# Kernel optimization log

Measured on AMD Instinct MI355X. Metric: run time of the kernel, lower is better.

Reference implementation:

```python
import jax, jax.numpy as jnp
import numpy as np

N = 100_000      # nodes
E = 1_200_000    # edges (before self-loops)
F_IN = 128       # num_node_features
G = 256          # number of graphs in the batch
C = 10           # num_classes
NEG_SLOPE = 0.2  # PyG GATConv default


def setup_inputs() -> dict:
    key = jax.random.key(0)
    ks = jax.random.split(key, 20)
    x = jax.random.normal(ks[0], (N, F_IN), jnp.float32)
    edge_index = jax.random.randint(ks[1], (2, E), 0, N, dtype=jnp.int32)
    # sorted graph assignment covering all G graphs (no empty segments)
    batch = (jnp.arange(N, dtype=jnp.int32) * G) // N

    def lin(k, fi, fo):
        return jax.random.normal(k, (fi, fo), jnp.float32) * (1.0 / np.sqrt(fi))

    dims = [(F_IN, 16), (16, 32), (32, 64)]
    params = {}
    for i, (fi, fo) in enumerate(dims, start=1):
        params[f"W{i}"] = lin(ks[3 * i], fi, fo)
        params[f"a{i}_src"] = jax.random.normal(ks[3 * i + 1], (fo,), jnp.float32) * 0.1
        params[f"a{i}_dst"] = jax.random.normal(ks[3 * i + 2], (fo,), jnp.float32) * 0.1
        params[f"b{i}"] = jnp.zeros((fo,), jnp.float32)
    params["fc_w"] = lin(ks[15], 64, C)
    params["fc_b"] = jnp.zeros((C,), jnp.float32)
    return {"x": x, "edge_index": edge_index, "batch": batch, **params}


def _gat_layer(x, src, dst, W, a_src, a_dst, b):
    # h = Theta x; e_ij = LeakyReLU(a_src.h_j + a_dst.h_i), softmax over dst i
    h = x @ W                                     # [N, F]
    s = h @ a_src                                 # [N]
    d = h @ a_dst                                 # [N]
    logits = jax.nn.leaky_relu(s[src] + d[dst], NEG_SLOPE)   # [E+N]
    m = jax.ops.segment_max(logits, dst, num_segments=N)     # per-dst max
    ex = jnp.exp(logits - m[dst])
    denom = jax.ops.segment_sum(ex, dst, num_segments=N)
    alpha = ex / (denom[dst] + 1e-16)             # [E+N]
    out = jax.ops.segment_sum(alpha[:, None] * h[src], dst, num_segments=N)
    return out + b


def reference(x, edge_index, batch, W1, a1_src, a1_dst, b1, W2, a2_src, a2_dst, b2,
              W3, a3_src, a3_dst, b3, fc_w, fc_b):
    # add self-loops (PyG GATConv default) -> every dst segment non-empty
    loops = jnp.arange(N, dtype=edge_index.dtype)
    src = jnp.concatenate([edge_index[0], loops])
    dst = jnp.concatenate([edge_index[1], loops])

    h = jax.nn.relu(_gat_layer(x, src, dst, W1, a1_src, a1_dst, b1))
    # F.dropout(training=False) is a no-op in eval
    h = jax.nn.relu(_gat_layer(h, src, dst, W2, a2_src, a2_dst, b2))
    h = jax.nn.relu(_gat_layer(h, src, dst, W3, a3_src, a3_dst, b3))
    pooled = jax.ops.segment_max(h, batch, num_segments=G)   # global_max_pool [G, 64]
    logits = pooled @ fc_w + fc_b
    return jax.nn.log_softmax(logits, axis=1)
```

## Files before the change

kernel.cpp:

```cpp
#include <hip/hip_runtime.h>
#include <hip/hip_bf16.h>
#include <hip/hip_fp16.h>
#include <math.h>

#define NEG_SLOPE 0.2f
#define NCHUNK 1024
#define BSHIFT 9
#define BNODES 512

__device__ __forceinline__ float leaky(float x) { return x > 0.f ? x : NEG_SLOPE * x; }
__device__ __forceinline__ int usan(int v, int n) { return ((unsigned)v < (unsigned)n) ? v : 0; }

__global__ void chunk_hist(const int* __restrict__ dst, int E, int Ec, int nbuck,
                           int* __restrict__ hmatT) {
    extern __shared__ int hist[];
    int c = blockIdx.x;
    for (int b = threadIdx.x; b < nbuck; b += 256) hist[b] = 0;
    __syncthreads();
    int lo = c * Ec, hi = min(E, lo + Ec);
    for (int e = lo + threadIdx.x; e < hi; e += 256) atomicAdd(&hist[dst[e] >> BSHIFT], 1);
    __syncthreads();
    for (int b = threadIdx.x; b < nbuck; b += 256) hmatT[b * NCHUNK + c] = hist[b];
}

// ... 67 lines not shown
    hist[t] = 0;
    __syncthreads();
    int lo = bbase[b], hi = bbase[b + 1];
    for (int j = lo + t; j < hi; j += BNODES) atomicAdd(&hist[bbuf[j] & (BNODES - 1)], 1);
    __syncthreads();
    int own = hist[t];
    for (int o = 1; o < BNODES; o <<= 1) {
        int add = (t >= o) ? hist[t - o] : 0;
        __syncthreads();
        hist[t] += add;
        __syncthreads();
    }
    int excl = hist[t] - own;
    int n = (b << BSHIFT) + t;
    int off_n = n + bbase[b] + excl;
    offl[t] = off_n;
    cur[t] = 0;
    if (n < N) {
        offs[n] = off_n;
        csr[off_n] = n;
    }
    __syncthreads();
    for (int j = lo + t; j < hi; j += BNODES) {
        int v = bbuf[j];
        int ld = v & (BNODES - 1);
        int r = atomicAdd(&cur[ld], 1);
        csr[offl[ld] + 1 + r] = v >> BSHIFT;
    }
}


template <int FIN, int FOUT>
__global__ void transform(const float* __restrict__ xin, const float* __restrict__ W,
                          const float* __restrict__ asrc, const float* __restrict__ adst,
                          __half* __restrict__ h, float* __restrict__ sv, float* __restrict__ dv,
                          int N) {
    constexpr int TPN = FOUT / 4;
    constexpr int BN  = 256 / TPN;
    constexpr int PITCH = FIN + 4;
    __shared__ float xs[BN * PITCH];
    __shared__ float wl[FIN * FOUT];
    __shared__ float al[FOUT], bl[FOUT];
    for (int j = threadIdx.x; j < FIN * FOUT; j += 256) wl[j] = W[j];
    if (threadIdx.x < FOUT) { al[threadIdx.x] = asrc[threadIdx.x]; bl[threadIdx.x] = adst[threadIdx.x]; }
    int base = blockIdx.x * BN;
    constexpr int NV = BN * FIN / 4;
    const float4* xg = (const float4*)xin + (size_t)base * (FIN / 4);
    int limv = ((N - base) * FIN) >> 2;
    for (int v = threadIdx.x; v < NV; v += 256) {
        int n = v / (FIN / 4), c = v % (FIN / 4);
        float4 val = (v < limv) ? xg[v] : make_float4(0.f, 0.f, 0.f, 0.f);
        *(float4*)&xs[n * PITCH + c * 4] = val;
    }
    __syncthreads();
    int node_l = threadIdx.x / TPN;
    int fq = (threadIdx.x % TPN) * 4;
    int node = base + node_l;
    const float* xrow = &xs[node_l * PITCH];
    float4 acc = make_float4(0.f, 0.f, 0.f, 0.f);
#pragma unroll 8
    for (int k = 0; k < FIN; k++) {
        float xv = xrow[k];
        float4 w4 = *(const float4*)&wl[k * FOUT + fq];
        acc.x += xv * w4.x; acc.y += xv * w4.y; acc.z += xv * w4.z; acc.w += xv * w4.w;
    }
    if (node < N) {
        __half2* hp = (__half2*)(h + (size_t)node * FOUT + fq);
        hp[0] = __floats2half2_rn(acc.x, acc.y);
        hp[1] = __floats2half2_rn(acc.z, acc.w);
        float sp = acc.x * al[fq] + acc.y * al[fq + 1] + acc.z * al[fq + 2] + acc.w * al[fq + 3];
        float dp = acc.x * bl[fq] + acc.y * bl[fq + 1] + acc.z * bl[fq + 2] + acc.w * bl[fq + 3];
#pragma unroll
        for (int o = TPN / 2; o > 0; o >>= 1) { sp += __shfl_xor(sp, o); dp += __shfl_xor(dp, o); }
        if (fq == 0) { sv[node] = sp; dv[node] = dp; }
    }
}


template <int FI, int FO>
__global__ void gat_trans(const __half* __restrict__ h, const float* __restrict__ sv,
                          const float* __restrict__ dv, const int* __restrict__ offs,
                          const int* __restrict__ csr, const float* __restrict__ bias,
                          const float* __restrict__ Wn, const float* __restrict__ an_s,
                          const float* __restrict__ an_d,
                          __half* __restrict__ h2, float* __restrict__ sv2,
                          float* __restrict__ dv2, int N) {
    constexpr int L  = FI / 8;
    constexpr int L2 = 2 * L;
    constexpr int CPL = FO / L2;
    constexpr int NPB = 256 / L2;
    __shared__ float wl[FI * FO];
    __shared__ float al[FO], bl[FO];
    for (int j = threadIdx.x; j < FI * FO; j += 256) wl[j] = Wn[j];
    if (threadIdx.x < FO) { al[threadIdx.x] = an_s[threadIdx.x]; bl[threadIdx.x] = an_d[threadIdx.x]; }
    __syncthreads();
    int lane  = threadIdx.x % L;
    int lane2 = threadIdx.x % L2;
    int half  = (threadIdx.x / L) & 1;
    int wlane = threadIdx.x & 63;
    int sgbase  = wlane & ~(L - 1);
    int grpbase = wlane & ~(L2 - 1);
    int i = blockIdx.x * NPB + threadIdx.x / L2;
    if (i >= N) return;
    int beg = offs[i], end = offs[i + 1];
    float di = dv[i];
    float acc[8];
#pragma unroll
    for (int c = 0; c < 8; c++) acc[c] = 0.f;
    float ssum = 0.f;
    const int k3 = lane & 3;

    int j0 = beg + 4 * half;
    int j1 = j0 + 8;
    bool vA = (j0 + 4 <= end);
    bool vB = (j1 + 4 <= end);
    int j0e = vA ? j0 : beg;
    int a0 = usan(csr[j0e], N),     a1 = usan(csr[j0e + 1], N);
    int a2 = usan(csr[j0e + 2], N), a3 = usan(csr[j0e + 3], N);
    uint4 uA0 = *((const uint4*)(h + (size_t)a0 * FI) + lane);
    uint4 uA1 = *((const uint4*)(h + (size_t)a1 * FI) + lane);
    uint4 uA2 = *((const uint4*)(h + (size_t)a2 * FI) + lane);
    uint4 uA3 = *((const uint4*)(h + (size_t)a3 * FI) + lane);
    float svA, svA2 = 0.f;
    if constexpr (L >= 4) {
        int sel = a0;
        if (k3 == 1) sel = a1; else if (k3 == 2) sel = a2; else if (k3 == 3) sel = a3;
        svA = sv[sel];
    } else {
        svA  = sv[lane ? a1 : a0];
        svA2 = sv[lane ? a3 : a2];
    }
    int j1e = vB ? j1 : beg;
    int b0 = usan(csr[j1e], N),     b1 = usan(csr[j1e + 1], N);
    int b2 = usan(csr[j1e + 2], N), b3 = usan(csr[j1e + 3], N);
    while (vA) {
        int j2 = j1 + 8;
        bool vC = vB && (j2 + 4 <= end);
        uint4 uB0 = *((const uint4*)(h + (size_t)b0 * FI) + lane);
        uint4 uB1 = *((const uint4*)(h + (size_t)b1 * FI) + lane);
        uint4 uB2 = *((const uint4*)(h + (size_t)b2 * FI) + lane);
        uint4 uB3 = *((const uint4*)(h + (size_t)b3 * FI) + lane);
        float svB, svB2 = 0.f;
        if constexpr (L >= 4) {
            int sel = b0;
            if (k3 == 1) sel = b1; else if (k3 == 2) sel = b2; else if (k3 == 3) sel = b3;
            svB = sv[sel];
        } else {
            svB  = sv[lane ? b1 : b0];
            svB2 = sv[lane ? b3 : b2];
        }
        int j2e = vC ? j2 : beg;
        int c0 = usan(csr[j2e], N),     c1 = usan(csr[j2e + 1], N);
        int c2 = usan(csr[j2e + 2], N), c3 = usan(csr[j2e + 3], N);
        float w0, w1, w2, w3;
        if constexpr (L >= 4) {
            float myw = __expf(leaky(svA + di));
            w0 = __shfl(myw, sgbase + 0);
            w1 = __shfl(myw, sgbase + 1);
            w2 = __shfl(myw, sgbase + 2);
            w3 = __shfl(myw, sgbase + 3);
        } else {
            float mya = __expf(leaky(svA + di));
            float myb = __expf(leaky(svA2 + di));
            w0 = __shfl(mya, sgbase + 0);
            w1 = __shfl(mya, sgbase + 1);
            w2 = __shfl(myb, sgbase + 0);
            w3 = __shfl(myb, sgbase + 1);
        }
        ssum += (w0 + w1) + (w2 + w3);
#pragma unroll
        for (int c = 0; c < 4; c++) {
            float2 f0 = __half22float2(((const __half2*)&uA0)[c]);
            float2 f1 = __half22float2(((const __half2*)&uA1)[c]);
            float2 f2 = __half22float2(((const __half2*)&uA2)[c]);
            float2 f3 = __half22float2(((const __half2*)&uA3)[c]);
            acc[2 * c]     += w0 * f0.x + w1 * f1.x + w2 * f2.x + w3 * f3.x;
            acc[2 * c + 1] += w0 * f0.y + w1 * f1.y + w2 * f2.y + w3 * f3.y;
        }
        uA0 = uB0; uA1 = uB1; uA2 = uB2; uA3 = uB3;
        svA = svB; svA2 = svB2;
        b0 = c0; b1 = c1; b2 = c2; b3 = c3;
        j0 = j1; j1 = j2; vA = vB; vB = vC;
    }
    int rem = end - j0;
    if (rem > 0) {
        int o1 = rem > 1 ? 1 : 0;
        int o2 = rem > 2 ? 2 : o1;
        int t0 = usan(csr[j0], N), t1 = usan(csr[j0 + o1], N), t2 = usan(csr[j0 + o2], N);
        uint4 r0 = *((const uint4*)(h + (size_t)t0 * FI) + lane);
        uint4 r1 = *((const uint4*)(h + (size_t)t1 * FI) + lane);
        uint4 r2 = *((const uint4*)(h + (size_t)t2 * FI) + lane);
        float s0 = sv[t0], s1 = sv[t1], s2 = sv[t2];
        float w0t = __expf(leaky(s0 + di));
        float w1t = rem > 1 ? __expf(leaky(s1 + di)) : 0.f;
        float w2t = rem > 2 ? __expf(leaky(s2 + di)) : 0.f;
        ssum += w0t + w1t + w2t;
#pragma unroll
        for (int c = 0; c < 4; c++) {
            float2 f0 = __half22float2(((const __half2*)&r0)[c]);
            float2 f1 = __half22float2(((const __half2*)&r1)[c]);
            float2 f2 = __half22float2(((const __half2*)&r2)[c]);
            acc[2 * c]     += w0t * f0.x + w1t * f1.x + w2t * f2.x;
            acc[2 * c + 1] += w0t * f0.y + w1t * f1.y + w2t * f2.y;
        }
    }
#pragma unroll
    for (int c = 0; c < 8; c++) acc[c] += __shfl_xor(acc[c], L);
    ssum += __shfl_xor(ssum, L);

    float inv = 1.0f / ssum;
    float4 ba = ((const float4*)bias)[lane * 2];
    float4 bb = ((const float4*)bias)[lane * 2 + 1];
    float yv[8];
    yv[0] = fmaxf(acc[0] * inv + ba.x, 0.f);
    yv[1] = fmaxf(acc[1] * inv + ba.y, 0.f);
    yv[2] = fmaxf(acc[2] * inv + ba.z, 0.f);
    yv[3] = fmaxf(acc[3] * inv + ba.w, 0.f);
    yv[4] = fmaxf(acc[4] * inv + bb.x, 0.f);
    yv[5] = fmaxf(acc[5] * inv + bb.y, 0.f);
    yv[6] = fmaxf(acc[6] * inv + bb.z, 0.f);
    yv[7] = fmaxf(acc[7] * inv + bb.w, 0.f);
    int colbase = lane2 * CPL;
    float oacc[CPL];
#pragma unroll
    for (int c = 0; c < CPL; c++) oacc[c] = 0.f;
#pragma unroll
    for (int jj = 0; jj < L; jj++) {
        float v[8];
#pragma unroll
        for (int r = 0; r < 8; r++) v[r] = __shfl(yv[r], grpbase + jj);
#pragma unroll
        for (int r = 0; r < 8; r++) {
            const float* wrow = &wl[(jj * 8 + r) * FO + colbase];
#pragma unroll
            for (int c = 0; c < CPL; c++) oacc[c] += v[r] * wrow[c];
        }
    }
    __half2 hp[CPL / 2];
#pragma unroll
    for (int c = 0; c < CPL / 2; c++) hp[c] = __floats2half2_rn(oacc[2 * c], oacc[2 * c + 1]);
    *((uint4*)(h2 + (size_t)i * FO + colbase)) = *(uint4*)&hp[0];
    float sp = 0.f, dp = 0.f;
#pragma unroll
    for (int c = 0; c < CPL; c++) { sp += oacc[c] * al[colbase + c]; dp += oacc[c] * bl[colbase + c]; }
#pragma unroll
    for (int o = 1; o < L2; o <<= 1) { sp += __shfl_xor(sp, o); dp += __shfl_xor(dp, o); }
    if (lane2 == 0) { sv2[i] = sp; dv2[i] = dp; }
}


template <int F>
__global__ void gat_fused(const __half* __restrict__ h, const float* __restrict__ sv,
                          const float* __restrict__ dv, const int* __restrict__ offs,
                          const int* __restrict__ csr, const float* __restrict__ bias,
                          __half* __restrict__ y, int N) {
    constexpr int L  = F / 8;
    constexpr int L2 = 2 * L;
    constexpr int NPB = 256 / L2;
    int lane  = threadIdx.x % L;
    int half  = (threadIdx.x / L) & 1;
    int wlane = threadIdx.x & 63;
    int sgbase = wlane & ~(L - 1);
    int i = blockIdx.x * NPB + threadIdx.x / L2;
    if (i >= N) return;
    int beg = offs[i], end = offs[i + 1];
    float di = dv[i];
    float acc[8];
#pragma unroll
    for (int c = 0; c < 8; c++) acc[c] = 0.f;
    float ssum = 0.f;
    const int k3 = lane & 3;

    int j0 = beg + 4 * half;
    int j1 = j0 + 8;
    bool vA = (j0 + 4 <= end);
    bool vB = (j1 + 4 <= end);
    int j0e = vA ? j0 : beg;
    int a0 = usan(csr[j0e], N),     a1 = usan(csr[j0e + 1], N);
    int a2 = usan(csr[j0e + 2], N), a3 = usan(csr[j0e + 3], N);
    uint4 uA0 = *((const uint4*)(h + (size_t)a0 * F) + lane);
    uint4 uA1 = *((const uint4*)(h + (size_t)a1 * F) + lane);
    uint4 uA2 = *((const uint4*)(h + (size_t)a2 * F) + lane);
    uint4 uA3 = *((const uint4*)(h + (size_t)a3 * F) + lane);
    int sel = a0;
    if (k3 == 1) sel = a1; else if (k3 == 2) sel = a2; else if (k3 == 3) sel = a3;
    float svA = sv[sel];
    int j1e = vB ? j1 : beg;
    int b0 = usan(csr[j1e], N),     b1 = usan(csr[j1e + 1], N);
    int b2 = usan(csr[j1e + 2], N), b3 = usan(csr[j1e + 3], N);
    while (vA) {
        int j2 = j1 + 8;
        bool vC = vB && (j2 + 4 <= end);
        uint4 uB0 = *((const uint4*)(h + (size_t)b0 * F) + lane);
        uint4 uB1 = *((const uint4*)(h + (size_t)b1 * F) + lane);
        uint4 uB2 = *((const uint4*)(h + (size_t)b2 * F) + lane);
        uint4 uB3 = *((const uint4*)(h + (size_t)b3 * F) + lane);
        int selB = b0;
        if (k3 == 1) selB = b1; else if (k3 == 2) selB = b2; else if (k3 == 3) selB = b3;
        float svB = sv[selB];
        int j2e = vC ? j2 : beg;
        int c0 = usan(csr[j2e], N),     c1 = usan(csr[j2e + 1], N);
        int c2 = usan(csr[j2e + 2], N), c3 = usan(csr[j2e + 3], N);
        float myw = __expf(leaky(svA + di));
        float w0 = __shfl(myw, sgbase + 0);
        float w1 = __shfl(myw, sgbase + 1);
        float w2 = __shfl(myw, sgbase + 2);
        float w3 = __shfl(myw, sgbase + 3);
        ssum += (w0 + w1) + (w2 + w3);
#pragma unroll
        for (int c = 0; c < 4; c++) {
            float2 f0 = __half22float2(((const __half2*)&uA0)[c]);
            float2 f1 = __half22float2(((const __half2*)&uA1)[c]);
            float2 f2 = __half22float2(((const __half2*)&uA2)[c]);
            float2 f3 = __half22float2(((const __half2*)&uA3)[c]);
            acc[2 * c]     += w0 * f0.x + w1 * f1.x + w2 * f2.x + w3 * f3.x;
            acc[2 * c + 1] += w0 * f0.y + w1 * f1.y + w2 * f2.y + w3 * f3.y;
        }
        uA0 = uB0; uA1 = uB1; uA2 = uB2; uA3 = uB3;
        svA = svB;
        b0 = c0; b1 = c1; b2 = c2; b3 = c3;
        j0 = j1; j1 = j2; vA = vB; vB = vC;
    }
    int rem = end - j0;
    if (rem > 0) {
        int o1 = rem > 1 ? 1 : 0;
        int o2 = rem > 2 ? 2 : o1;
        int t0 = usan(csr[j0], N), t1 = usan(csr[j0 + o1], N), t2 = usan(csr[j0 + o2], N);
        uint4 r0 = *((const uint4*)(h + (size_t)t0 * F) + lane);
        uint4 r1 = *((const uint4*)(h + (size_t)t1 * F) + lane);
        uint4 r2 = *((const uint4*)(h + (size_t)t2 * F) + lane);
        float s0 = sv[t0], s1 = sv[t1], s2 = sv[t2];
        float w0t = __expf(leaky(s0 + di));
        float w1t = rem > 1 ? __expf(leaky(s1 + di)) : 0.f;
        float w2t = rem > 2 ? __expf(leaky(s2 + di)) : 0.f;
        ssum += w0t + w1t + w2t;
#pragma unroll
        for (int c = 0; c < 4; c++) {
            float2 f0 = __half22float2(((const __half2*)&r0)[c]);
            float2 f1 = __half22float2(((const __half2*)&r1)[c]);
            float2 f2 = __half22float2(((const __half2*)&r2)[c]);
            acc[2 * c]     += w0t * f0.x + w1t * f1.x + w2t * f2.x;
            acc[2 * c + 1] += w0t * f0.y + w1t * f1.y + w2t * f2.y;
        }
    }
#pragma unroll
    for (int c = 0; c < 8; c++) acc[c] += __shfl_xor(acc[c], L);
    ssum += __shfl_xor(ssum, L);
    if (half == 0) {
        float inv = 1.0f / ssum;
        float4 ba = ((const float4*)bias)[lane * 2];
        float4 bb = ((const float4*)bias)[lane * 2 + 1];
        __half2 o[4];
        o[0] = __floats2half2_rn(fmaxf(acc[0] * inv + ba.x, 0.f), fmaxf(acc[1] * inv + ba.y, 0.f));
        o[1] = __floats2half2_rn(fmaxf(acc[2] * inv + ba.z, 0.f), fmaxf(acc[3] * inv + ba.w, 0.f));
        o[2] = __floats2half2_rn(fmaxf(acc[4] * inv + bb.x, 0.f), fmaxf(acc[5] * inv + bb.y, 0.f));
        o[3] = __floats2half2_rn(fmaxf(acc[6] * inv + bb.z, 0.f), fmaxf(acc[7] * inv + bb.w, 0.f));
        ((uint4*)(y + (size_t)i * F))[lane] = *(uint4*)&o[0];
    }
}


__global__ void pool_head(const __half* __restrict__ y, const float* __restrict__ fcw,
                          const float* __restrict__ fcb, float* __restrict__ out,
                          int N, int G, int C) {
    __shared__ float red[256];
    __shared__ float pl[64];
    int g = blockIdx.x;
    long long gl = g;
    int start = (int)((gl * N + G - 1) / G);
    int end = (int)(((gl + 1) * N + G - 1) / G);
    int f = threadIdx.x & 63, w = threadIdx.x >> 6;
    float m = 0.f;
    for (int i = start + w; i < end; i += 4) m = fmaxf(m, __half2float(y[(size_t)i * 64 + f]));
    red[threadIdx.x] = m;
    __syncthreads();
    if (threadIdx.x < 64) {
        pl[f] = fmaxf(fmaxf(red[f], red[64 + f]), fmaxf(red[128 + f], red[192 + f]));
    }
    __syncthreads();
    if (threadIdx.x < 64) {
        int c = threadIdx.x;
        float z = -1e30f;
        if (c < C) {
            z = fcb[c];
            for (int k = 0; k < 64; k++) z += pl[k] * fcw[k * 10 + c];
        }
        float zm = z;
#pragma unroll
        for (int o = 1; o < 16; o <<= 1) zm = fmaxf(zm, __shfl_xor(zm, o));
        float e = (c < C) ? __expf(z - zm) : 0.f;
// ... 12 lines not shown
    const int*   eidx = (const int*)d_in[1];
    const float* W1 = (const float*)d_in[3];
    const float* a1s = (const float*)d_in[4];
    const float* a1d = (const float*)d_in[5];
    const float* b1 = (const float*)d_in[6];
    const float* W2 = (const float*)d_in[7];
    const float* a2s = (const float*)d_in[8];
    const float* a2d = (const float*)d_in[9];
    const float* b2 = (const float*)d_in[10];
    const float* W3 = (const float*)d_in[11];
    const float* a3s = (const float*)d_in[12];
    const float* a3d = (const float*)d_in[13];
    const float* b3 = (const float*)d_in[14];
    const float* fcw = (const float*)d_in[15];
    const float* fcb = (const float*)d_in[16];
    float* out = (float*)d_out;

    const int N = in_sizes[2];
    const int E = in_sizes[1] / 2;
    const int C = in_sizes[16];
    const int G = out_size / C;

    const int* src = eidx;
    const int* dst = eidx + E;

    size_t off = 0;
    auto alloc = [&](size_t bytes) -> void* {
        void* p = (char*)d_ws + off;
        off += (bytes + 255) & ~(size_t)255;
        return p;
    };
    int* offs   = (int*)alloc((size_t)(N + 1) * 4);
    int* csr    = (int*)alloc((size_t)(E + N) * 4 + 256);
    float* sbufA = (float*)alloc((size_t)N * 4);
    float* dbufA = (float*)alloc((size_t)N * 4);
    float* sbufB = (float*)alloc((size_t)N * 4);
    float* dbufB = (float*)alloc((size_t)N * 4);
    __half* hA = (__half*)alloc((size_t)N * 64 * 2);
    __half* hB = (__half*)alloc((size_t)N * 64 * 2);

    const int NBUCK = (N + BNODES - 1) >> BSHIFT;
    const int Ec = (E + NCHUNK - 1) / NCHUNK;
    int* hmatT = (int*)alloc((size_t)NBUCK * NCHUNK * 4);
    int* btot  = (int*)alloc((size_t)NBUCK * 4);
    int* bbase = (int*)alloc((size_t)(NBUCK + 1) * 4);
    int* bbuf  = (int*)hB;

    const size_t histBytes = (size_t)NBUCK * 4;

    chunk_hist<<<NCHUNK, 256, histBytes, stream>>>(dst, E, Ec, NBUCK, hmatT);
    mat_scan<<<NBUCK, 256, 0, stream>>>(hmatT, btot);
    base_scan<<<1, 256, 0, stream>>>(btot, NBUCK, bbase, offs, N, E);
    chunk_scatter<<<NCHUNK, 256, histBytes, stream>>>(src, dst, E, Ec, NBUCK, hmatT, bbase, bbuf);
    bucket_build<<<NBUCK, BNODES, 0, stream>>>(bbase, bbuf, N, offs, csr);

    transform<128, 16><<<(N + 63) / 64, 256, 0, stream>>>(x, W1, a1s, a1d, hA, sbufA, dbufA, N);
    gat_trans<16, 32><<<(N + 63) / 64, 256, 0, stream>>>(hA, sbufA, dbufA, offs, csr, b1,
                                                         W2, a2s, a2d, hB, sbufB, dbufB, N);
    gat_trans<32, 64><<<(N + 31) / 32, 256, 0, stream>>>(hB, sbufB, dbufB, offs, csr, b2,
                                                         W3, a3s, a3d, hA, sbufA, dbufA, N);
    gat_fused<64><<<(N + 15) / 16, 256, 0, stream>>>(hA, sbufA, dbufA, offs, csr, b3, hB, N);

    pool_head<<<G, 256, 0, stream>>>(hB, fcw, fcb, out, N, G, C);
}
```

Measured before the change: 265.9 us.

## Split wide GAT aggregations into 16-feature planes for cache-resident gathers

Feature matrices for layers 2 and 3 are stored as separate 16-column half planes, so each aggregation pass gathers rows from a 3.2MB plane instead of the full wide matrix. Layer 2 runs as two plane passes, with the second also applying the layer-3 linear transform. Layer 3 runs as four plane passes. The aim is for the random neighbor gathers to hit in L2/LLC more often. In exchange the CSR, attention scalars and softmax weights are re-read and recomputed once per plane pass, and there are more kernel launches.

After: 320.6 us. 20.6% more time.

```diff
diff --git a/kernel.cpp b/kernel.cpp
--- a/kernel.cpp
+++ b/kernel.cpp
@@ -174,8 +174,8 @@
                           const int* __restrict__ csr, const float* __restrict__ bias,
                           const float* __restrict__ Wn, const float* __restrict__ an_s,
                           const float* __restrict__ an_d,
-                          __half* __restrict__ h2, float* __restrict__ sv2,
-                          float* __restrict__ dv2, int N) {
+                          __half* __restrict__ h2lo, __half* __restrict__ h2hi,
+                          float* __restrict__ sv2, float* __restrict__ dv2, int N) {
     constexpr int L  = FI / 8;
     constexpr int L2 = 2 * L;
     constexpr int CPL = FO / L2;
@@ -199,7 +199,6 @@
 #pragma unroll
     for (int c = 0; c < 8; c++) acc[c] = 0.f;
     float ssum = 0.f;
-    const int k3 = lane & 3;
 
     int j0 = beg + 4 * half;
     int j1 = j0 + 8;
@@ -212,15 +211,8 @@
     uint4 uA1 = *((const uint4*)(h + (size_t)a1 * FI) + lane);
     uint4 uA2 = *((const uint4*)(h + (size_t)a2 * FI) + lane);
     uint4 uA3 = *((const uint4*)(h + (size_t)a3 * FI) + lane);
-    float svA, svA2 = 0.f;
-    if constexpr (L >= 4) {
-        int sel = a0;
-        if (k3 == 1) sel = a1; else if (k3 == 2) sel = a2; else if (k3 == 3) sel = a3;
-        svA = sv[sel];
-    } else {
-        svA  = sv[lane ? a1 : a0];
-        svA2 = sv[lane ? a3 : a2];
-    }
+    float svA  = sv[lane ? a1 : a0];
+    float svA2 = sv[lane ? a3 : a2];
     int j1e = vB ? j1 : beg;
     int b0 = usan(csr[j1e], N),     b1 = usan(csr[j1e + 1], N);
     int b2 = usan(csr[j1e + 2], N), b3 = usan(csr[j1e + 3], N);
@@ -231,33 +223,17 @@
         uint4 uB1 = *((const uint4*)(h + (size_t)b1 * FI) + lane);
         uint4 uB2 = *((const uint4*)(h + (size_t)b2 * FI) + lane);
         uint4 uB3 = *((const uint4*)(h + (size_t)b3 * FI) + lane);
-        float svB, svB2 = 0.f;
-        if constexpr (L >= 4) {
-            int sel = b0;
-            if (k3 == 1) sel = b1; else if (k3 == 2) sel = b2; else if (k3 == 3) sel = b3;
-            svB = sv[sel];
-        } else {
-            svB  = sv[lane ? b1 : b0];
-            svB2 = sv[lane ? b3 : b2];
-        }
+        float svB  = sv[lane ? b1 : b0];
+        float svB2 = sv[lane ? b3 : b2];
         int j2e = vC ? j2 : beg;
         int c0 = usan(csr[j2e], N),     c1 = usan(csr[j2e + 1], N);
         int c2 = usan(csr[j2e + 2], N), c3 = usan(csr[j2e + 3], N);
-        float w0, w1, w2, w3;
-        if constexpr (L >= 4) {
-            float myw = __expf(leaky(svA + di));
-            w0 = __shfl(myw, sgbase + 0);
-            w1 = __shfl(myw, sgbase + 1);
-            w2 = __shfl(myw, sgbase + 2);
-            w3 = __shfl(myw, sgbase + 3);
-        } else {
-            float mya = __expf(leaky(svA + di));
-            float myb = __expf(leaky(svA2 + di));
-            w0 = __shfl(mya, sgbase + 0);
-            w1 = __shfl(mya, sgbase + 1);
-            w2 = __shfl(myb, sgbase + 0);
-            w3 = __shfl(myb, sgbase + 1);
-        }
+        float mya = __expf(leaky(svA + di));
+        float myb = __expf(leaky(svA2 + di));
+        float w0 = __shfl(mya, sgbase + 0);
+        float w1 = __shfl(mya, sgbase + 1);
+        float w2 = __shfl(myb, sgbase + 0);
+        float w3 = __shfl(myb, sgbase + 1);
         ssum += (w0 + w1) + (w2 + w3);
 #pragma unroll
         for (int c = 0; c < 4; c++) {
@@ -330,7 +306,9 @@
     __half2 hp[CPL / 2];
 #pragma unroll
     for (int c = 0; c < CPL / 2; c++) hp[c] = __floats2half2_rn(oacc[2 * c], oacc[2 * c + 1]);
-    *((uint4*)(h2 + (size_t)i * FO + colbase)) = *(uint4*)&hp[0];
+    __half* dstp = (colbase < 16) ? (h2lo + (size_t)i * 16 + colbase)
+                                  : (h2hi + (size_t)i * 16 + (colbase - 16));
+    *(uint4*)dstp = *(uint4*)&hp[0];
     float sp = 0.f, dp = 0.f;
 #pragma unroll
     for (int c = 0; c < CPL; c++) { sp += oacc[c] * al[colbase + c]; dp += oacc[c] * bl[colbase + c]; }
@@ -340,18 +318,30 @@
 }
 
 
-template <int F>
-__global__ void gat_fused(const __half* __restrict__ h, const float* __restrict__ sv,
+template <int MODE>
+__global__ void gat_plane(const __half* __restrict__ hp, const float* __restrict__ sv,
                           const float* __restrict__ dv, const int* __restrict__ offs,
                           const int* __restrict__ csr, const float* __restrict__ bias,
-                          __half* __restrict__ y, int N) {
-    constexpr int L  = F / 8;
-    constexpr int L2 = 2 * L;
-    constexpr int NPB = 256 / L2;
+                          __half* __restrict__ yout, const __half* __restrict__ ylo,
+                          const float* __restrict__ Wn, const float* __restrict__ an_s,
+                          const float* __restrict__ an_d, __half* __restrict__ h3p,
+                          float* __restrict__ sv2, float* __restrict__ dv2, int N) {
+    constexpr int L = 2, L2 = 4, NPB = 64;
+    constexpr int YSTRIDE = (MODE == 0) ? 64 : 16;
+    __shared__ float wl[(MODE == 2) ? 32 * 64 : 1];
+    __shared__ float al[(MODE == 2) ? 64 : 1];
+    __shared__ float bl[(MODE == 2) ? 64 : 1];
+    if constexpr (MODE == 2) {
+        for (int j = threadIdx.x; j < 32 * 64; j += 256) wl[j] = Wn[j];
+        if (threadIdx.x < 64) { al[threadIdx.x] = an_s[threadIdx.x]; bl[threadIdx.x] = an_d[threadIdx.x]; }
+        __syncthreads();
+    }
     int lane  = threadIdx.x % L;
+    int lane2 = threadIdx.x % L2;
     int half  = (threadIdx.x / L) & 1;
     int wlane = threadIdx.x & 63;
-    int sgbase = wlane & ~(L - 1);
+    int sgbase  = wlane & ~(L - 1);
+    int grpbase = wlane & ~(L2 - 1);
     int i = blockIdx.x * NPB + threadIdx.x / L2;
     if (i >= N) return;
     int beg = offs[i], end = offs[i + 1];
@@ -360,7 +350,6 @@
 #pragma unroll
     for (int c = 0; c < 8; c++) acc[c] = 0.f;
     float ssum = 0.f;
-    const int k3 = lane & 3;
 
     int j0 = beg + 4 * half;
     int j1 = j0 + 8;
@@ -369,34 +358,33 @@
     int j0e = vA ? j0 : beg;
     int a0 = usan(csr[j0e], N),     a1 = usan(csr[j0e + 1], N);
     int a2 = usan(csr[j0e + 2], N), a3 = usan(csr[j0e + 3], N);
-    uint4 uA0 = *((const uint4*)(h + (size_t)a0 * F) + lane);
-    uint4 uA1 = *((const uint4*)(h + (size_t)a1 * F) + lane);
-    uint4 uA2 = *((const uint4*)(h + (size_t)a2 * F) + lane);
-    uint4 uA3 = *((const uint4*)(h + (size_t)a3 * F) + lane);
-    int sel = a0;
-    if (k3 == 1) sel = a1; else if (k3 == 2) sel = a2; else if (k3 == 3) sel = a3;
-    float svA = sv[sel];
+    uint4 uA0 = *((const uint4*)(hp + (size_t)a0 * 16) + lane);
+    uint4 uA1 = *((const uint4*)(hp + (size_t)a1 * 16) + lane);
+    uint4 uA2 = *((const uint4*)(hp + (size_t)a2 * 16) + lane);
+    uint4 uA3 = *((const uint4*)(hp + (size_t)a3 * 16) + lane);
+    float svA  = sv[lane ? a1 : a0];
+    float svA2 = sv[lane ? a3 : a2];
     int j1e = vB ? j1 : beg;
     int b0 = usan(csr[j1e], N),     b1 = usan(csr[j1e + 1], N);
     int b2 = usan(csr[j1e + 2], N), b3 = usan(csr[j1e + 3], N);
     while (vA) {
         int j2 = j1 + 8;
         bool vC = vB && (j2 + 4 <= end);
-        uint4 uB0 = *((const uint4*)(h + (size_t)b0 * F) + lane);
-        uint4 uB1 = *((const uint4*)(h + (size_t)b1 * F) + lane);
-        uint4 uB2 = *((const uint4*)(h + (size_t)b2 * F) + lane);
-        uint4 uB3 = *((const uint4*)(h + (size_t)b3 * F) + lane);
-        int selB = b0;
-        if (k3 == 1) selB = b1; else if (k3 == 2) selB = b2; else if (k3 == 3) selB = b3;
-        float svB = sv[selB];
+        uint4 uB0 = *((const uint4*)(hp + (size_t)b0 * 16) + lane);
+        uint4 uB1 = *((const uint4*)(hp + (size_t)b1 * 16) + lane);
+        uint4 uB2 = *((const uint4*)(hp + (size_t)b2 * 16) + lane);
+        uint4 uB3 = *((const uint4*)(hp + (size_t)b3 * 16) + lane);
+        float svB  = sv[lane ? b1 : b0];
+        float svB2 = sv[lane ? b3 : b2];
         int j2e = vC ? j2 : beg;
         int c0 = usan(csr[j2e], N),     c1 = usan(csr[j2e + 1], N);
         int c2 = usan(csr[j2e + 2], N), c3 = usan(csr[j2e + 3], N);
-        float myw = __expf(leaky(svA + di));
-        float w0 = __shfl(myw, sgbase + 0);
-        float w1 = __shfl(myw, sgbase + 1);
-        float w2 = __shfl(myw, sgbase + 2);
-        float w3 = __shfl(myw, sgbase + 3);
+        float mya = __expf(leaky(svA + di));
+        float myb = __expf(leaky(svA2 + di));
+        float w0 = __shfl(mya, sgbase + 0);
+        float w1 = __shfl(mya, sgbase + 1);
+        float w2 = __shfl(myb, sgbase + 0);
+        float w3 = __shfl(myb, sgbase + 1);
         ssum += (w0 + w1) + (w2 + w3);
 #pragma unroll
         for (int c = 0; c < 4; c++) {
@@ -408,7 +396,7 @@
             acc[2 * c + 1] += w0 * f0.y + w1 * f1.y + w2 * f2.y + w3 * f3.y;
         }
         uA0 = uB0; uA1 = uB1; uA2 = uB2; uA3 = uB3;
-        svA = svB;
+        svA = svB; svA2 = svB2;
         b0 = c0; b1 = c1; b2 = c2; b3 = c3;
         j0 = j1; j1 = j2; vA = vB; vB = vC;
     }
@@ -417,9 +405,9 @@
         int o1 = rem > 1 ? 1 : 0;
         int o2 = rem > 2 ? 2 : o1;
         int t0 = usan(csr[j0], N), t1 = usan(csr[j0 + o1], N), t2 = usan(csr[j0 + o2], N);
-        uint4 r0 = *((const uint4*)(h + (size_t)t0 * F) + lane);
-        uint4 r1 = *((const uint4*)(h + (size_t)t1 * F) + lane);
-        uint4 r2 = *((const uint4*)(h + (size_t)t2 * F) + lane);
+        uint4 r0 = *((const uint4*)(hp + (size_t)t0 * 16) + lane);
+        uint4 r1 = *((const uint4*)(hp + (size_t)t1 * 16) + lane);
+        uint4 r2 = *((const uint4*)(hp + (size_t)t2 * 16) + lane);
         float s0 = sv[t0], s1 = sv[t1], s2 = sv[t2];
         float w0t = __expf(leaky(s0 + di));
         float w1t = rem > 1 ? __expf(leaky(s1 + di)) : 0.f;
@@ -437,16 +425,68 @@
 #pragma unroll
     for (int c = 0; c < 8; c++) acc[c] += __shfl_xor(acc[c], L);
     ssum += __shfl_xor(ssum, L);
-    if (half == 0) {
-        float inv = 1.0f / ssum;
-        float4 ba = ((const float4*)bias)[lane * 2];
-        float4 bb = ((const float4*)bias)[lane * 2 + 1];
-        __half2 o[4];
-        o[0] = __floats2half2_rn(fmaxf(acc[0] * inv + ba.x, 0.f), fmaxf(acc[1] * inv + ba.y, 0.f));
-        o[1] = __floats2half2_rn(fmaxf(acc[2] * inv + ba.z, 0.f), fmaxf(acc[3] * inv + ba.w, 0.f));
-        o[2] = __floats2half2_rn(fmaxf(acc[4] * inv + bb.x, 0.f), fmaxf(acc[5] * inv + bb.y, 0.f));
-        o[3] = __floats2half2_rn(fmaxf(acc[6] * inv + bb.z, 0.f), fmaxf(acc[7] * inv + bb.w, 0.f));
-        ((uint4*)(y + (size_t)i * F))[lane] = *(uint4*)&o[0];
+    float inv = 1.0f / ssum;
+
+    if constexpr (MODE == 0 || MODE == 1) {
+        if (half == 0) {
+            float4 ba = ((const float4*)bias)[lane * 2];
+            float4 bb = ((const float4*)bias)[lane * 2 + 1];
+            __half2 o[4];
+            o[0] = __floats2half2_rn(fmaxf(acc[0] * inv + ba.x, 0.f), fmaxf(acc[1] * inv + ba.y, 0.f));
+            o[1] = __floats2half2_rn(fmaxf(acc[2] * inv + ba.z, 0.f), fmaxf(acc[3] * inv + ba.w, 0.f));
+            o[2] = __floats2half2_rn(fmaxf(acc[4] * inv + bb.x, 0.f), fmaxf(acc[5] * inv + bb.y, 0.f));
+            o[3] = __floats2half2_rn(fmaxf(acc[6] * inv + bb.z, 0.f), fmaxf(acc[7] * inv + bb.w, 0.f));
+            *(uint4*)(yout + (size_t)i * YSTRIDE + lane * 8) = *(uint4*)&o[0];
+        }
+    } else {
+        float yv[8];
+        if (lane2 < 2) {
+            uint4 u = *(const uint4*)(ylo + (size_t)i * 16 + lane2 * 8);
+#pragma unroll
+            for (int c = 0; c < 4; c++) {
+                float2 f = __half22float2(((const __half2*)&u)[c]);
+                yv[2 * c] = f.x; yv[2 * c + 1] = f.y;
+            }
+        } else {
+            float4 ba = ((const float4*)bias)[(lane2 - 2) * 2];
+            float4 bb = ((const float4*)bias)[(lane2 - 2) * 2 + 1];
+            yv[0] = fmaxf(acc[0] * inv + ba.x, 0.f);
+            yv[1] = fmaxf(acc[1] * inv + ba.y, 0.f);
+            yv[2] = fmaxf(acc[2] * inv + ba.z, 0.f);
+            yv[3] = fmaxf(acc[3] * inv + ba.w, 0.f);
+            yv[4] = fmaxf(acc[4] * inv + bb.x, 0.f);
+            yv[5] = fmaxf(acc[5] * inv + bb.y, 0.f);
+            yv[6] = fmaxf(acc[6] * inv + bb.z, 0.f);
+            yv[7] = fmaxf(acc[7] * inv + bb.w, 0.f);
+        }
+        int colbase = lane2 * 16;
+        float oacc[16];
+#pragma unroll
+        for (int c = 0; c < 16; c++) oacc[c] = 0.f;
+#pragma unroll
+        for (int q = 0; q < 4; q++) {
+            float v[8];
+#pragma unroll
+            for (int r = 0; r < 8; r++) v[r] = __shfl(yv[r], grpbase + q);
+#pragma unroll
+            for (int r = 0; r < 8; r++) {
+                const float* wrow = &wl[(q * 8 + r) * 64 + colbase];
+#pragma unroll
+                for (int c = 0; c < 16; c++) oacc[c] += v[r] * wrow[c];
+            }
+        }
+        __half2 hh[8];
+#pragma unroll
+        for (int c = 0; c < 8; c++) hh[c] = __floats2half2_rn(oacc[2 * c], oacc[2 * c + 1]);
+        __half* dpp = h3p + (size_t)lane2 * ((size_t)N * 16) + (size_t)i * 16;
+        *(uint4*)dpp       = *(uint4*)&hh[0];
+        *(uint4*)(dpp + 8) = *(uint4*)&hh[4];
+        float sp = 0.f, dq = 0.f;
+#pragma unroll
+        for (int c = 0; c < 16; c++) { sp += oacc[c] * al[colbase + c]; dq += oacc[c] * bl[colbase + c]; }
+#pragma unroll
+        for (int o = 1; o < 4; o <<= 1) { sp += __shfl_xor(sp, o); dq += __shfl_xor(dq, o); }
+        if (lane2 == 0) { sv2[i] = sp; dv2[i] = dq; }
     }
 }
 
@@ -529,15 +569,19 @@
     float* dbufA = (float*)alloc((size_t)N * 4);
     float* sbufB = (float*)alloc((size_t)N * 4);
     float* dbufB = (float*)alloc((size_t)N * 4);
-    __half* hA = (__half*)alloc((size_t)N * 64 * 2);
-    __half* hB = (__half*)alloc((size_t)N * 64 * 2);
+    __half* h1   = (__half*)alloc((size_t)N * 16 * 2);
+    __half* h2lo = (__half*)alloc((size_t)N * 16 * 2);
+    __half* h2hi = (__half*)alloc((size_t)N * 16 * 2);
+    __half* y2lo = (__half*)alloc((size_t)N * 16 * 2);
+    __half* h3p  = (__half*)alloc((size_t)N * 64 * 2);
+    __half* y    = (__half*)alloc((size_t)N * 64 * 2);
 
     const int NBUCK = (N + BNODES - 1) >> BSHIFT;
     const int Ec = (E + NCHUNK - 1) / NCHUNK;
     int* hmatT = (int*)alloc((size_t)NBUCK * NCHUNK * 4);
     int* btot  = (int*)alloc((size_t)NBUCK * 4);
     int* bbase = (int*)alloc((size_t)(NBUCK + 1) * 4);
-    int* bbuf  = (int*)hB;
+    int* bbuf  = (int*)y;
 
     const size_t histBytes = (size_t)NBUCK * 4;
 
@@ -547,12 +591,21 @@
     chunk_scatter<<<NCHUNK, 256, histBytes, stream>>>(src, dst, E, Ec, NBUCK, hmatT, bbase, bbuf);
     bucket_build<<<NBUCK, BNODES, 0, stream>>>(bbase, bbuf, N, offs, csr);
 
-    transform<128, 16><<<(N + 63) / 64, 256, 0, stream>>>(x, W1, a1s, a1d, hA, sbufA, dbufA, N);
-    gat_trans<16, 32><<<(N + 63) / 64, 256, 0, stream>>>(hA, sbufA, dbufA, offs, csr, b1,
-                                                         W2, a2s, a2d, hB, sbufB, dbufB, N);
-    gat_trans<32, 64><<<(N + 31) / 32, 256, 0, stream>>>(hB, sbufB, dbufB, offs, csr, b2,
-                                                         W3, a3s, a3d, hA, sbufA, dbufA, N);
-    gat_fused<64><<<(N + 15) / 16, 256, 0, stream>>>(hA, sbufA, dbufA, offs, csr, b3, hB, N);
-
-    pool_head<<<G, 256, 0, stream>>>(hB, fcw, fcb, out, N, G, C);
-}
+    const int GRID = (N + 63) / 64;
+
+    transform<128, 16><<<GRID, 256, 0, stream>>>(x, W1, a1s, a1d, h1, sbufA, dbufA, N);
+    gat_trans<16, 32><<<GRID, 256, 0, stream>>>(h1, sbufA, dbufA, offs, csr, b1,
+                                                W2, a2s, a2d, h2lo, h2hi, sbufB, dbufB, N);
+    gat_plane<1><<<GRID, 256, 0, stream>>>(h2lo, sbufB, dbufB, offs, csr, b2,
+                                           y2lo, nullptr, nullptr, nullptr, nullptr,
+                                           nullptr, nullptr, nullptr, N);
+    gat_plane<2><<<GRID, 256, 0, stream>>>(h2hi, sbufB, dbufB, offs, csr, b2 + 16,
+                                           nullptr, y2lo, W3, a3s, a3d, h3p, sbufA, dbufA, N);
+    for (int P = 0; P < 4; P++) {
+        gat_plane<0><<<GRID, 256, 0, stream>>>(h3p + (size_t)P * N * 16, sbufA, dbufA, offs, csr,
+                                               b3 + P * 16, y + P * 16, nullptr,
+                                               nullptr, nullptr, nullptr, nullptr, nullptr, nullptr, N);
+    }
+
+    pool_head<<<G, 256, 0, stream>>>(y, fcw, fcb, out, N, G, C);
+}
```

## Recompute source attention scores from gathered features instead of loading per-node buffer

Applied to the files above, without the earlier changes.

Drops the precomputed per-node source score arrays. Each edge kernel now computes a_src·h_j on the fly from the half-precision feature row it already gathers, using lane dot products and xor-shuffle reductions. This removes one scattered 4-byte gather per edge and the writes of the score buffers. In exchange it adds per-edge FMA and shuffle work, and the scores now come from fp16-rounded features rather than full-precision ones, which slightly changes the numerics.

Result: slower. 274.5 us (+3.2%).

```diff
diff --git a/kernel.cpp b/kernel.cpp
--- a/kernel.cpp
+++ b/kernel.cpp
@@ -123,17 +123,16 @@
 
 template <int FIN, int FOUT>
 __global__ void transform(const float* __restrict__ xin, const float* __restrict__ W,
-                          const float* __restrict__ asrc, const float* __restrict__ adst,
-                          __half* __restrict__ h, float* __restrict__ sv, float* __restrict__ dv,
-                          int N) {
+                          const float* __restrict__ adst,
+                          __half* __restrict__ h, float* __restrict__ dv, int N) {
     constexpr int TPN = FOUT / 4;
     constexpr int BN  = 256 / TPN;
     constexpr int PITCH = FIN + 4;
     __shared__ float xs[BN * PITCH];
     __shared__ float wl[FIN * FOUT];
-    __shared__ float al[FOUT], bl[FOUT];
+    __shared__ float bl[FOUT];
     for (int j = threadIdx.x; j < FIN * FOUT; j += 256) wl[j] = W[j];
-    if (threadIdx.x < FOUT) { al[threadIdx.x] = asrc[threadIdx.x]; bl[threadIdx.x] = adst[threadIdx.x]; }
+    if (threadIdx.x < FOUT) bl[threadIdx.x] = adst[threadIdx.x];
     int base = blockIdx.x * BN;
     constexpr int NV = BN * FIN / 4;
     const float4* xg = (const float4*)xin + (size_t)base * (FIN / 4);
@@ -159,47 +158,45 @@
         __half2* hp = (__half2*)(h + (size_t)node * FOUT + fq);
         hp[0] = __floats2half2_rn(acc.x, acc.y);
         hp[1] = __floats2half2_rn(acc.z, acc.w);
-        float sp = acc.x * al[fq] + acc.y * al[fq + 1] + acc.z * al[fq + 2] + acc.w * al[fq + 3];
         float dp = acc.x * bl[fq] + acc.y * bl[fq + 1] + acc.z * bl[fq + 2] + acc.w * bl[fq + 3];
 #pragma unroll
-        for (int o = TPN / 2; o > 0; o >>= 1) { sp += __shfl_xor(sp, o); dp += __shfl_xor(dp, o); }
-        if (fq == 0) { sv[node] = sp; dv[node] = dp; }
+        for (int o = TPN / 2; o > 0; o >>= 1) dp += __shfl_xor(dp, o);
+        if (fq == 0) dv[node] = dp;
     }
 }
 
 
 template <int FI, int FO>
-__global__ void gat_trans(const __half* __restrict__ h, const float* __restrict__ sv,
+__global__ void gat_trans(const __half* __restrict__ h, const float* __restrict__ asrc,
                           const float* __restrict__ dv, const int* __restrict__ offs,
                           const int* __restrict__ csr, const float* __restrict__ bias,
-                          const float* __restrict__ Wn, const float* __restrict__ an_s,
-                          const float* __restrict__ an_d,
-                          __half* __restrict__ h2, float* __restrict__ sv2,
-                          float* __restrict__ dv2, int N) {
+                          const float* __restrict__ Wn, const float* __restrict__ an_d,
+                          __half* __restrict__ h2, float* __restrict__ dv2, int N) {
     constexpr int L  = FI / 8;
     constexpr int L2 = 2 * L;
     constexpr int CPL = FO / L2;
     constexpr int NPB = 256 / L2;
     __shared__ float wl[FI * FO];
-    __shared__ float al[FO], bl[FO];
+    __shared__ float bl[FO];
     for (int j = threadIdx.x; j < FI * FO; j += 256) wl[j] = Wn[j];
-    if (threadIdx.x < FO) { al[threadIdx.x] = an_s[threadIdx.x]; bl[threadIdx.x] = an_d[threadIdx.x]; }
+    if (threadIdx.x < FO) bl[threadIdx.x] = an_d[threadIdx.x];
     __syncthreads();
     int lane  = threadIdx.x % L;
     int lane2 = threadIdx.x % L2;
+    int wlane = threadIdx.x & 63;
     int half  = (threadIdx.x / L) & 1;
-    int wlane = threadIdx.x & 63;
-    int sgbase  = wlane & ~(L - 1);
     int grpbase = wlane & ~(L2 - 1);
     int i = blockIdx.x * NPB + threadIdx.x / L2;
     if (i >= N) return;
+    float asr[8];
+#pragma unroll
+    for (int k = 0; k < 8; k++) asr[k] = asrc[lane * 8 + k];
     int beg = offs[i], end = offs[i + 1];
     float di = dv[i];
     float acc[8];
 #pragma unroll
     for (int c = 0; c < 8; c++) acc[c] = 0.f;
     float ssum = 0.f;
-    const int k3 = lane & 3;
 
     int j0 = beg + 4 * half;
     int j1 = j0 + 8;
@@ -212,15 +209,6 @@
     uint4 uA1 = *((const uint4*)(h + (size_t)a1 * FI) + lane);
     uint4 uA2 = *((const uint4*)(h + (size_t)a2 * FI) + lane);
     uint4 uA3 = *((const uint4*)(h + (size_t)a3 * FI) + lane);
-    float svA, svA2 = 0.f;
-    if constexpr (L >= 4) {
-        int sel = a0;
-        if (k3 == 1) sel = a1; else if (k3 == 2) sel = a2; else if (k3 == 3) sel = a3;
-        svA = sv[sel];
-    } else {
-        svA  = sv[lane ? a1 : a0];
-        svA2 = sv[lane ? a3 : a2];
-    }
     int j1e = vB ? j1 : beg;
     int b0 = usan(csr[j1e], N),     b1 = usan(csr[j1e + 1], N);
     int b2 = usan(csr[j1e + 2], N), b3 = usan(csr[j1e + 3], N);
@@ -231,45 +219,41 @@
         uint4 uB1 = *((const uint4*)(h + (size_t)b1 * FI) + lane);
         uint4 uB2 = *((const uint4*)(h + (size_t)b2 * FI) + lane);
         uint4 uB3 = *((const uint4*)(h + (size_t)b3 * FI) + lane);
-        float svB, svB2 = 0.f;
-        if constexpr (L >= 4) {
-            int sel = b0;
-            if (k3 == 1) sel = b1; else if (k3 == 2) sel = b2; else if (k3 == 3) sel = b3;
-            svB = sv[sel];
-        } else {
-            svB  = sv[lane ? b1 : b0];
-            svB2 = sv[lane ? b3 : b2];
-        }
         int j2e = vC ? j2 : beg;
         int c0 = usan(csr[j2e], N),     c1 = usan(csr[j2e + 1], N);
         int c2 = usan(csr[j2e + 2], N), c3 = usan(csr[j2e + 3], N);
-        float w0, w1, w2, w3;
-        if constexpr (L >= 4) {
-            float myw = __expf(leaky(svA + di));
-            w0 = __shfl(myw, sgbase + 0);
-            w1 = __shfl(myw, sgbase + 1);
-            w2 = __shfl(myw, sgbase + 2);
-            w3 = __shfl(myw, sgbase + 3);
-        } else {
-            float mya = __expf(leaky(svA + di));
-            float myb = __expf(leaky(svA2 + di));
-            w0 = __shfl(mya, sgbase + 0);
-            w1 = __shfl(mya, sgbase + 1);
-            w2 = __shfl(myb, sgbase + 0);
-            w3 = __shfl(myb, sgbase + 1);
-        }
+        float2 f0[4], f1[4], f2[4], f3[4];
+#pragma unroll
+        for (int c = 0; c < 4; c++) {
+            f0[c] = __half22float2(((const __half2*)&uA0)[c]);
+            f1[c] = __half22float2(((const __half2*)&uA1)[c]);
+            f2[c] = __half22float2(((const __half2*)&uA2)[c]);
+            f3[c] = __half22float2(((const __half2*)&uA3)[c]);
+        }
+        float p0 = 0.f, p1 = 0.f, p2 = 0.f, p3 = 0.f;
+#pragma unroll
+        for (int c = 0; c < 4; c++) {
+            p0 += f0[c].x * asr[2 * c] + f0[c].y * asr[2 * c + 1];
+            p1 += f1[c].x * asr[2 * c] + f1[c].y * asr[2 * c + 1];
+            p2 += f2[c].x * asr[2 * c] + f2[c].y * asr[2 * c + 1];
+            p3 += f3[c].x * asr[2 * c] + f3[c].y * asr[2 * c + 1];
+        }
+#pragma unroll
+        for (int o = 1; o < L; o <<= 1) {
+            p0 += __shfl_xor(p0, o); p1 += __shfl_xor(p1, o);
+            p2 += __shfl_xor(p2, o); p3 += __shfl_xor(p3, o);
+        }
+        float w0 = __expf(leaky(p0 + di));
+        float w1 = __expf(leaky(p1 + di));
+        float w2 = __expf(leaky(p2 + di));
+        float w3 = __expf(leaky(p3 + di));
         ssum += (w0 + w1) + (w2 + w3);
 #pragma unroll
         for (int c = 0; c < 4; c++) {
-            float2 f0 = __half22float2(((const __half2*)&uA0)[c]);
-            float2 f1 = __half22float2(((const __half2*)&uA1)[c]);
-            float2 f2 = __half22float2(((const __half2*)&uA2)[c]);
-            float2 f3 = __half22float2(((const __half2*)&uA3)[c]);
-            acc[2 * c]     += w0 * f0.x + w1 * f1.x + w2 * f2.x + w3 * f3.x;
-            acc[2 * c + 1] += w0 * f0.y + w1 * f1.y + w2 * f2.y + w3 * f3.y;
+            acc[2 * c]     += w0 * f0[c].x + w1 * f1[c].x + w2 * f2[c].x + w3 * f3[c].x;
+            acc[2 * c + 1] += w0 * f0[c].y + w1 * f1[c].y + w2 * f2[c].y + w3 * f3[c].y;
         }
         uA0 = uB0; uA1 = uB1; uA2 = uB2; uA3 = uB3;
-        svA = svB; svA2 = svB2;
         b0 = c0; b1 = c1; b2 = c2; b3 = c3;
         j0 = j1; j1 = j2; vA = vB; vB = vC;
     }
@@ -281,18 +265,32 @@
         uint4 r0 = *((const uint4*)(h + (size_t)t0 * FI) + lane);
         uint4 r1 = *((const uint4*)(h + (size_t)t1 * FI) + lane);
         uint4 r2 = *((const uint4*)(h + (size_t)t2 * FI) + lane);
-        float s0 = sv[t0], s1 = sv[t1], s2 = sv[t2];
-        float w0t = __expf(leaky(s0 + di));
-        float w1t = rem > 1 ? __expf(leaky(s1 + di)) : 0.f;
-        float w2t = rem > 2 ? __expf(leaky(s2 + di)) : 0.f;
+        float2 g0[4], g1[4], g2[4];
+#pragma unroll
+        for (int c = 0; c < 4; c++) {
+            g0[c] = __half22float2(((const __half2*)&r0)[c]);
+            g1[c] = __half22float2(((const __half2*)&r1)[c]);
+            g2[c] = __half22float2(((const __half2*)&r2)[c]);
+        }
+        float q0 = 0.f, q1 = 0.f, q2 = 0.f;
+#pragma unroll
+        for (int c = 0; c < 4; c++) {
+            q0 += g0[c].x * asr[2 * c] + g0[c].y * asr[2 * c + 1];
+            q1 += g1[c].x * asr[2 * c] + g1[c].y * asr[2 * c + 1];
+            q2 += g2[c].x * asr[2 * c] + g2[c].y * asr[2 * c + 1];
+        }
+#pragma unroll
+        for (int o = 1; o < L; o <<= 1) {
+            q0 += __shfl_xor(q0, o); q1 += __shfl_xor(q1, o); q2 += __shfl_xor(q2, o);
+        }
+        float w0t = __expf(leaky(q0 + di));
+        float w1t = rem > 1 ? __expf(leaky(q1 + di)) : 0.f;
+        float w2t = rem > 2 ? __expf(leaky(q2 + di)) : 0.f;
         ssum += w0t + w1t + w2t;
 #pragma unroll
         for (int c = 0; c < 4; c++) {
-            float2 f0 = __half22float2(((const __half2*)&r0)[c]);
-            float2 f1 = __half22float2(((const __half2*)&r1)[c]);
-            float2 f2 = __half22float2(((const __half2*)&r2)[c]);
-            acc[2 * c]     += w0t * f0.x + w1t * f1.x + w2t * f2.x;
-            acc[2 * c + 1] += w0t * f0.y + w1t * f1.y + w2t * f2.y;
+            acc[2 * c]     += w0t * g0[c].x + w1t * g1[c].x + w2t * g2[c].x;
+            acc[2 * c + 1] += w0t * g0[c].y + w1t * g1[c].y + w2t * g2[c].y;
         }
     }
 #pragma unroll
@@ -331,17 +329,17 @@
 #pragma unroll
     for (int c = 0; c < CPL / 2; c++) hp[c] = __floats2half2_rn(oacc[2 * c], oacc[2 * c + 1]);
     *((uint4*)(h2 + (size_t)i * FO + colbase)) = *(uint4*)&hp[0];
-    float sp = 0.f, dp = 0.f;
-#pragma unroll
-    for (int c = 0; c < CPL; c++) { sp += oacc[c] * al[colbase + c]; dp += oacc[c] * bl[colbase + c]; }
-#pragma unroll
-    for (int o = 1; o < L2; o <<= 1) { sp += __shfl_xor(sp, o); dp += __shfl_xor(dp, o); }
-    if (lane2 == 0) { sv2[i] = sp; dv2[i] = dp; }
+    float dp = 0.f;
+#pragma unroll
+    for (int c = 0; c < CPL; c++) dp += oacc[c] * bl[colbase + c];
+#pragma unroll
+    for (int o = 1; o < L2; o <<= 1) dp += __shfl_xor(dp, o);
+    if (lane2 == 0) dv2[i] = dp;
 }
 
 
 template <int F>
-__global__ void gat_fused(const __half* __restrict__ h, const float* __restrict__ sv,
+__global__ void gat_fused(const __half* __restrict__ h, const float* __restrict__ asrc,
                           const float* __restrict__ dv, const int* __restrict__ offs,
                           const int* __restrict__ csr, const float* __restrict__ bias,
                           __half* __restrict__ y, int N) {
@@ -350,17 +348,17 @@
     constexpr int NPB = 256 / L2;
     int lane  = threadIdx.x % L;
     int half  = (threadIdx.x / L) & 1;
-    int wlane = threadIdx.x & 63;
-    int sgbase = wlane & ~(L - 1);
     int i = blockIdx.x * NPB + threadIdx.x / L2;
     if (i >= N) return;
+    float asr[8];
+#pragma unroll
+    for (int k = 0; k < 8; k++) asr[k] = asrc[lane * 8 + k];
     int beg = offs[i], end = offs[i + 1];
     float di = dv[i];
     float acc[8];
 #pragma unroll
     for (int c = 0; c < 8; c++) acc[c] = 0.f;
     float ssum = 0.f;
-    const int k3 = lane & 3;
 
     int j0 = beg + 4 * half;
     int j1 = j0 + 8;
@@ -373,9 +371,6 @@
     uint4 uA1 = *((const uint4*)(h + (size_t)a1 * F) + lane);
     uint4 uA2 = *((const uint4*)(h + (size_t)a2 * F) + lane);
     uint4 uA3 = *((const uint4*)(h + (size_t)a3 * F) + lane);
-    int sel = a0;
-    if (k3 == 1) sel = a1; else if (k3 == 2) sel = a2; else if (k3 == 3) sel = a3;
-    float svA = sv[sel];
     int j1e = vB ? j1 : beg;
     int b0 = usan(csr[j1e], N),     b1 = usan(csr[j1e + 1], N);
     int b2 = usan(csr[j1e + 2], N), b3 = usan(csr[j1e + 3], N);
@@ -386,29 +381,41 @@
         uint4 uB1 = *((const uint4*)(h + (size_t)b1 * F) + lane);
         uint4 uB2 = *((const uint4*)(h + (size_t)b2 * F) + lane);
         uint4 uB3 = *((const uint4*)(h + (size_t)b3 * F) + lane);
-        int selB = b0;
-        if (k3 == 1) selB = b1; else if (k3 == 2) selB = b2; else if (k3 == 3) selB = b3;
-        float svB = sv[selB];
         int j2e = vC ? j2 : beg;
         int c0 = usan(csr[j2e], N),     c1 = usan(csr[j2e + 1], N);
         int c2 = usan(csr[j2e + 2], N), c3 = usan(csr[j2e + 3], N);
-        float myw = __expf(leaky(svA + di));
-        float w0 = __shfl(myw, sgbase + 0);
-        float w1 = __shfl(myw, sgbase + 1);
-        float w2 = __shfl(myw, sgbase + 2);
-        float w3 = __shfl(myw, sgbase + 3);
+        float2 f0[4], f1[4], f2[4], f3[4];
+#pragma unroll
+        for (int c = 0; c < 4; c++) {
+            f0[c] = __half22float2(((const __half2*)&uA0)[c]);
+            f1[c] = __half22float2(((const __half2*)&uA1)[c]);
+            f2[c] = __half22float2(((const __half2*)&uA2)[c]);
+            f3[c] = __half22float2(((const __half2*)&uA3)[c]);
+        }
+        float p0 = 0.f, p1 = 0.f, p2 = 0.f, p3 = 0.f;
+#pragma unroll
+        for (int c = 0; c < 4; c++) {
+            p0 += f0[c].x * asr[2 * c] + f0[c].y * asr[2 * c + 1];
+            p1 += f1[c].x * asr[2 * c] + f1[c].y * asr[2 * c + 1];
+            p2 += f2[c].x * asr[2 * c] + f2[c].y * asr[2 * c + 1];
+            p3 += f3[c].x * asr[2 * c] + f3[c].y * asr[2 * c + 1];
+        }
+#pragma unroll
+        for (int o = 1; o < L; o <<= 1) {
+            p0 += __shfl_xor(p0, o); p1 += __shfl_xor(p1, o);
+            p2 += __shfl_xor(p2, o); p3 += __shfl_xor(p3, o);
+        }
+        float w0 = __expf(leaky(p0 + di));
+        float w1 = __expf(leaky(p1 + di));
+        float w2 = __expf(leaky(p2 + di));
+        float w3 = __expf(leaky(p3 + di));
         ssum += (w0 + w1) + (w2 + w3);
 #pragma unroll
         for (int c = 0; c < 4; c++) {
-            float2 f0 = __half22float2(((const __half2*)&uA0)[c]);
-            float2 f1 = __half22float2(((const __half2*)&uA1)[c]);
-            float2 f2 = __half22float2(((const __half2*)&uA2)[c]);
-            float2 f3 = __half22float2(((const __half2*)&uA3)[c]);
-            acc[2 * c]     += w0 * f0.x + w1 * f1.x + w2 * f2.x + w3 * f3.x;
-            acc[2 * c + 1] += w0 * f0.y + w1 * f1.y + w2 * f2.y + w3 * f3.y;
+            acc[2 * c]     += w0 * f0[c].x + w1 * f1[c].x + w2 * f2[c].x + w3 * f3[c].x;
+            acc[2 * c + 1] += w0 * f0[c].y + w1 * f1[c].y + w2 * f2[c].y + w3 * f3[c].y;
         }
         uA0 = uB0; uA1 = uB1; uA2 = uB2; uA3 = uB3;
-        svA = svB;
         b0 = c0; b1 = c1; b2 = c2; b3 = c3;
         j0 = j1; j1 = j2; vA = vB; vB = vC;
     }
@@ -420,18 +427,32 @@
         uint4 r0 = *((const uint4*)(h + (size_t)t0 * F) + lane);
         uint4 r1 = *((const uint4*)(h + (size_t)t1 * F) + lane);
         uint4 r2 = *((const uint4*)(h + (size_t)t2 * F) + lane);
-        float s0 = sv[t0], s1 = sv[t1], s2 = sv[t2];
-        float w0t = __expf(leaky(s0 + di));
-        float w1t = rem > 1 ? __expf(leaky(s1 + di)) : 0.f;
-        float w2t = rem > 2 ? __expf(leaky(s2 + di)) : 0.f;
+        float2 g0[4], g1[4], g2[4];
+#pragma unroll
+        for (int c = 0; c < 4; c++) {
+            g0[c] = __half22float2(((const __half2*)&r0)[c]);
+            g1[c] = __half22float2(((const __half2*)&r1)[c]);
+            g2[c] = __half22float2(((const __half2*)&r2)[c]);
+        }
+        float q0 = 0.f, q1 = 0.f, q2 = 0.f;
+#pragma unroll
+        for (int c = 0; c < 4; c++) {
+            q0 += g0[c].x * asr[2 * c] + g0[c].y * asr[2 * c + 1];
+            q1 += g1[c].x * asr[2 * c] + g1[c].y * asr[2 * c + 1];
+            q2 += g2[c].x * asr[2 * c] + g2[c].y * asr[2 * c + 1];
+        }
+#pragma unroll
+        for (int o = 1; o < L; o <<= 1) {
+            q0 += __shfl_xor(q0, o); q1 += __shfl_xor(q1, o); q2 += __shfl_xor(q2, o);
+        }
+        float w0t = __expf(leaky(q0 + di));
+        float w1t = rem > 1 ? __expf(leaky(q1 + di)) : 0.f;
+        float w2t = rem > 2 ? __expf(leaky(q2 + di)) : 0.f;
         ssum += w0t + w1t + w2t;
 #pragma unroll
         for (int c = 0; c < 4; c++) {
-            float2 f0 = __half22float2(((const __half2*)&r0)[c]);
-            float2 f1 = __half22float2(((const __half2*)&r1)[c]);
-            float2 f2 = __half22float2(((const __half2*)&r2)[c]);
-            acc[2 * c]     += w0t * f0.x + w1t * f1.x + w2t * f2.x;
-            acc[2 * c + 1] += w0t * f0.y + w1t * f1.y + w2t * f2.y;
+            acc[2 * c]     += w0t * g0[c].x + w1t * g1[c].x + w2t * g2[c].x;
+            acc[2 * c + 1] += w0t * g0[c].y + w1t * g1[c].y + w2t * g2[c].y;
         }
     }
 #pragma unroll
@@ -525,9 +546,7 @@
     };
     int* offs   = (int*)alloc((size_t)(N + 1) * 4);
     int* csr    = (int*)alloc((size_t)(E + N) * 4 + 256);
-    float* sbufA = (float*)alloc((size_t)N * 4);
     float* dbufA = (float*)alloc((size_t)N * 4);
-    float* sbufB = (float*)alloc((size_t)N * 4);
     float* dbufB = (float*)alloc((size_t)N * 4);
     __half* hA = (__half*)alloc((size_t)N * 64 * 2);
     __half* hB = (__half*)alloc((size_t)N * 64 * 2);
@@ -547,12 +566,12 @@
     chunk_scatter<<<NCHUNK, 256, histBytes, stream>>>(src, dst, E, Ec, NBUCK, hmatT, bbase, bbuf);
     bucket_build<<<NBUCK, BNODES, 0, stream>>>(bbase, bbuf, N, offs, csr);
 
-    transform<128, 16><<<(N + 63) / 64, 256, 0, stream>>>(x, W1, a1s, a1d, hA, sbufA, dbufA, N);
-    gat_trans<16, 32><<<(N + 63) / 64, 256, 0, stream>>>(hA, sbufA, dbufA, offs, csr, b1,
-                                                         W2, a2s, a2d, hB, sbufB, dbufB, N);
-    gat_trans<32, 64><<<(N + 31) / 32, 256, 0, stream>>>(hB, sbufB, dbufB, offs, csr, b2,
-                                                         W3, a3s, a3d, hA, sbufA, dbufA, N);
-    gat_fused<64><<<(N + 15) / 16, 256, 0, stream>>>(hA, sbufA, dbufA, offs, csr, b3, hB, N);
+    transform<128, 16><<<(N + 63) / 64, 256, 0, stream>>>(x, W1, a1d, hA, dbufA, N);
+    gat_trans<16, 32><<<(N + 63) / 64, 256, 0, stream>>>(hA, a1s, dbufA, offs, csr, b1,
+                                                         W2, a2d, hB, dbufB, N);
+    gat_trans<32, 64><<<(N + 31) / 32, 256, 0, stream>>>(hB, a2s, dbufB, offs, csr, b2,
+                                                         W3, a3d, hA, dbufA, N);
+    gat_fused<64><<<(N + 15) / 16, 256, 0, stream>>>(hA, a3s, dbufA, offs, csr, b3, hB, N);
 
     pool_head<<<G, 256, 0, stream>>>(hB, fcw, fcb, out, N, G, C);
 }
```
